# Kernel optimization log

Hardware: AMD Instinct MI355X
Metric: run time of the kernel (lower is better)

## Reference

```python
import jax, jax.numpy as jnp
import numpy as np

B = 32768
D_IN = 512
UNITS = 512


def setup_inputs() -> dict:
    key = jax.random.key(0)
    ks = jax.random.split(key, 12)
    s = 1.0 / np.sqrt(D_IN)
    sh = 1.0 / np.sqrt(UNITS)
    return {
        "inputs": jax.random.normal(ks[0], (B, D_IN), dtype=jnp.float32),
        "state": jax.random.normal(ks[1], (B, UNITS), dtype=jnp.float32),
        "att_score": jax.random.uniform(ks[2], (B, 1), dtype=jnp.float32),
        # update gate
        "Wu_x": jax.random.normal(ks[3], (D_IN, UNITS), dtype=jnp.float32) * s,
        "bu": jnp.zeros((UNITS,), dtype=jnp.float32),
        "Wu_h": jax.random.normal(ks[4], (UNITS, UNITS), dtype=jnp.float32) * sh,
        # reset gate
        "Wr_x": jax.random.normal(ks[5], (D_IN, UNITS), dtype=jnp.float32) * s,
        "br": jnp.zeros((UNITS,), dtype=jnp.float32),
        "Wr_h": jax.random.normal(ks[6], (UNITS, UNITS), dtype=jnp.float32) * sh,
        # candidate memory
        "Wc_x": jax.random.normal(ks[7], (D_IN, UNITS), dtype=jnp.float32) * s,
        "bc": jnp.zeros((UNITS,), dtype=jnp.float32),
        "Wc_h": jax.random.normal(ks[8], (UNITS, UNITS), dtype=jnp.float32) * sh,
    }


def reference(inputs, state, att_score, Wu_x, bu, Wu_h, Wr_x, br, Wr_h, Wc_x, bc, Wc_h):
    # u = sigmoid(Dense_act(x) + Dense_noact(h))
    u = jax.nn.sigmoid(inputs @ Wu_x + bu + state @ Wu_h)
    # r = sigmoid(Dense_act(x) + Dense_noact(h))
    r = jax.nn.sigmoid(inputs @ Wr_x + br + state @ Wr_h)
    # c = tanh(Dense_act(x) + r * Dense_noact(h))
    c = jnp.tanh(inputs @ Wc_x + bc + r * (state @ Wc_h))
    u_ = att_score * u  # [B,1] * [B,U] broadcast
    state_next = (1.0 - u_) * state + u_ * c
    return state_next
```

## Files before the change

### kernel.cpp

```cpp
#include <hip/hip_runtime.h>
#include <hip/hip_bf16.h>
#include <stdint.h>

#define B_ROWS 32768
#define DIM 512
#define THREADS 256
#define NKT 32
#define ABUF 8192
#define WBUF 12288
#define BUF (ABUF + WBUF)

typedef __attribute__((ext_vector_type(8))) __bf16 bf16x8;
typedef __attribute__((ext_vector_type(4))) float f32x4;
typedef __attribute__((ext_vector_type(4))) unsigned int uint4v;

__device__ static inline unsigned short f2bf(float f) {
    unsigned int u = __builtin_bit_cast(unsigned int, f);
    u += 0x7fffu + ((u >> 16) & 1u);
    return (unsigned short)(u >> 16);
}

__device__ static inline void load_lds_16B(const void* g, void* lds) {
    __builtin_amdgcn_global_load_lds(
        (const __attribute__((address_space(1))) unsigned int*)g,
        (__attribute__((address_space(3))) unsigned int*)lds,
        16, 0, 0);
}

__global__ void prep_weights(const float* __restrict__ Wu_x, const float* __restrict__ Wu_h,
                             const float* __restrict__ Wr_x, const float* __restrict__ Wr_h,
                             const float* __restrict__ Wc_x, const float* __restrict__ Wc_h,
                             unsigned short* __restrict__ Wt2) {
    __shared__ float tile[32][33];
    const int t = blockIdx.z;
    const int k0 = blockIdx.x * 32;
    const int n0 = blockIdx.y * 32;
    const float* Wx = (t == 0) ? Wu_x : (t == 1) ? Wr_x : Wc_x;
    const float* Wh = (t == 0) ? Wu_h : (t == 1) ? Wr_h : Wc_h;
    const int tid = threadIdx.x;
    const int c = tid & 31, r0 = tid >> 5;
#pragma unroll
    for (int i = 0; i < 4; ++i) {
        int kl = r0 + i * 8;
        int k = k0 + kl;
        int n = n0 + c;
        float v = (k < 512) ? Wx[(size_t)k * 512 + n] : Wh[(size_t)(k - 512) * 512 + n];
        tile[kl][c] = v;
    }
    __syncthreads();
    const int kt = k0 >> 5;
#pragma unroll
    for (int i = 0; i < 4; ++i) {
        int nl = r0 + i * 8;
        int kc = c;
        int n = n0 + nl;
        size_t base = (((size_t)kt * 3 + t) * 512 + n) * 64;
        *(unsigned short*)((char*)Wt2 + base + ((kc * 2) ^ (((n >> 1) & 3) << 4))) =
            f2bf(tile[kc][nl]);
    }
}

__global__ __launch_bounds__(THREADS, 2) void augru_main(
    const float* __restrict__ x, const float* __restrict__ h,
    const float* __restrict__ att, const unsigned short* __restrict__ Wt2,
    const float* __restrict__ bu, const float* __restrict__ br,
    const float* __restrict__ bc, float* __restrict__ out) {
    extern __shared__ char smem[];
    const int tid = threadIdx.x;
    const int lane = tid & 63;
    const int wid = tid >> 6;
    const int wm = wid >> 1;
    const int wn = wid & 1;
    const int id = blockIdx.x;
    const int wg = (id & 7) * 256 + (id >> 3);
    const int nb = wg & 7;
    const int mb = wg >> 3;
    const int cl = lane & 15;
    const int kg = lane >> 4;

    f32x4 accU[4][2], accR[4][2], accCx[4][2], accCh[4][2];
#pragma unroll
    for (int i = 0; i < 4; ++i)
#pragma unroll
        for (int j = 0; j < 2; ++j) {
            accU[i][j] = (f32x4)(0.f);
            accR[i][j] = (f32x4)(0.f);
            accCx[i][j] = (f32x4)(0.f);
            accCh[i][j] = (f32x4)(0.f);
        }

    const int rowb = wm * 64 + cl;
    const int aBase = rowb * 64 + ((kg * 16) ^ (((rowb >> 1) & 3) << 4));
    const int colb = wn * 32 + cl;
    const int wBase = ABUF + colb * 64 + ((kg * 16) ^ (((colb >> 1) & 3) << 4));

    const int arow = tid >> 1;
    const int ap = tid & 1;
    const int asw = ((arow >> 1) & 3) << 4;
    const int dsA0 = arow * 64 + ((ap * 32) ^ asw);
    const int dsA1 = arow * 64 + ((ap * 32 + 16) ^ asw);
    const float* pAx = x + (size_t)(mb * 128 + arow) * 512 + ap * 16;
    const float* pAh = h + (size_t)(mb * 128 + arow) * 512 - 512 + ap * 16;

    const char* gW0 = (const char*)Wt2 + ((size_t)nb * 64) * 64 + tid * 16;
    auto stageW = [&](int buf, int kt) {
        char* base = smem + buf * BUF;
        const char* gW = gW0 + (size_t)kt * (3 * 512 * 64);
#pragma unroll
        for (int t = 0; t < 3; ++t)
            load_lds_16B(gW + (size_t)t * (512 * 64),
                         base + ABUF + t * 4096 + wid * 1024);
    };

    f32x4 fa0, fa1, fa2, fa3;
    auto issueA = [&](int ktn) {
        const float* g = ((ktn < 16) ? pAx : pAh) + ktn * 32;
        asm volatile(
            "global_load_dwordx4 %0, %4, off\n\t"
            "global_load_dwordx4 %1, %4, off offset:16\n\t"
            "global_load_dwordx4 %2, %4, off offset:32\n\t"
            "global_load_dwordx4 %3, %4, off offset:48"
            : "=&v"(fa0), "=&v"(fa1), "=&v"(fa2), "=&v"(fa3)
            : "v"(g)
            : "memory");
    };

    auto cvt2 = [](float lo, float hi) {
        unsigned int r;
        asm("v_cvt_pk_bf16_f32 %0, %1, %2" : "=v"(r) : "v"(lo), "v"(hi));
        return r;
    };

    auto convertA = [&](int bufA, bool wLive) {
        if (wLive) asm volatile("s_waitcnt vmcnt(3)" ::: "memory");
        else       asm volatile("s_waitcnt vmcnt(0)" ::: "memory");
        __builtin_amdgcn_sched_barrier(0);
        uint4v q0, q1;
        q0.x = cvt2(fa0[0], fa0[1]); q0.y = cvt2(fa0[2], fa0[3]);
        q0.z = cvt2(fa1[0], fa1[1]); q0.w = cvt2(fa1[2], fa1[3]);
        q1.x = cvt2(fa2[0], fa2[1]); q1.y = cvt2(fa2[2], fa2[3]);
        q1.z = cvt2(fa3[0], fa3[1]); q1.w = cvt2(fa3[2], fa3[3]);
        char* base = smem + bufA * BUF;
        *(uint4v*)(base + dsA0) = q0;
        *(uint4v*)(base + dsA1) = q1;
    };

    stageW(0, 0);
    stageW(1, 1);
    stageW(2, 2);
    issueA(0);
    convertA(0, false);

    auto body = [&](int kt, int buf, int bufA, f32x4(&accC)[4][2]) {
        asm volatile("s_waitcnt lgkmcnt(0)" ::: "memory");
        __builtin_amdgcn_s_barrier();
        const bool doA = (kt + 1 < NKT);
        const bool doW = (kt + 3 < NKT);
        if (doA) issueA(kt + 1);
        if (doW) stageW((kt + 3) & 3, kt + 3);
        const char* aB = smem + buf * BUF;
        bf16x8 a[4], bb[3][2];
#pragma unroll
        for (int mi = 0; mi < 4; ++mi)
            a[mi] = __builtin_bit_cast(bf16x8,
                *(const uint4v*)(aB + aBase + mi * 1024));
#pragma unroll
        for (int t = 0; t < 3; ++t)
#pragma unroll
            for (int ni = 0; ni < 2; ++ni)
                bb[t][ni] = __builtin_bit_cast(bf16x8,
                    *(const uint4v*)(aB + wBase + t * 4096 + ni * 1024));
        __builtin_amdgcn_s_setprio(1);
#pragma unroll
        for (int ni = 0; ni < 2; ++ni) {
#pragma unroll
            for (int mi = 0; mi < 4; ++mi)
                accU[mi][ni] = __builtin_amdgcn_mfma_f32_16x16x32_bf16(
                    a[mi], bb[0][ni], accU[mi][ni], 0, 0, 0);
#pragma unroll
            for (int mi = 0; mi < 4; ++mi)
                accR[mi][ni] = __builtin_amdgcn_mfma_f32_16x16x32_bf16(
                    a[mi], bb[1][ni], accR[mi][ni], 0, 0, 0);
#pragma unroll
            for (int mi = 0; mi < 4; ++mi)
                accC[mi][ni] = __builtin_amdgcn_mfma_f32_16x16x32_bf16(
                    a[mi], bb[2][ni], accC[mi][ni], 0, 0, 0);
        }
        __builtin_amdgcn_s_setprio(0);
        if (doA) convertA(bufA, doW);
    };

    for (int g = 0; g < 4; ++g) {
        const int k0 = g * 4;
        body(k0 + 0, 0, 1, accCx);
        body(k0 + 1, 1, 2, accCx);
        body(k0 + 2, 2, 3, accCx);
        body(k0 + 3, 3, 0, accCx);
    }
    for (int g = 4; g < 8; ++g) {
        const int k0 = g * 4;
        body(k0 + 0, 0, 1, accCh);
        body(k0 + 1, 1, 2, accCh);
        body(k0 + 2, 2, 3, accCh);
        body(k0 + 3, 3, 0, accCh);
    }

#pragma unroll
    for (int ni = 0; ni < 2; ++ni) {
        const int col = nb * 64 + wn * 32 + ni * 16 + cl;
        const float bU = bu[col];
        const float bR = br[col];
        const float bC = bc[col];
#pragma unroll
        for (int mi = 0; mi < 4; ++mi) {
#pragma unroll
            for (int j = 0; j < 4; ++j) {
                const int row = mb * 128 + wm * 64 + mi * 16 + kg * 4 + j;
                const float up = accU[mi][ni][j] + bU;
                const float rp = accR[mi][ni][j] + bR;
                const float u = 1.f / (1.f + __expf(-up));
                const float r = 1.f / (1.f + __expf(-rp));
                const float cpre = accCx[mi][ni][j] + bC + r * accCh[mi][ni][j];
                const float e = __expf(-2.f * cpre);
                const float cc = (1.f - e) / (1.f + e);
                const float aa = att[row];
                const float hv = h[(size_t)row * 512 + col];
                const float u_ = aa * u;
                out[(size_t)row * 512 + col] = (1.f - u_) * hv + u_ * cc;
            }
        }
    }
}

extern "C" void kernel_launch(void* const* d_in, const int* in_sizes, int n_in,
                              void* d_out, int out_size, void* d_ws, size_t ws_size,
                              hipStream_t stream) {
    const float* x    = (const float*)d_in[0];
    const float* h    = (const float*)d_in[1];
    const float* att  = (const float*)d_in[2];
    const float* Wu_x = (const float*)d_in[3];
    const float* bu   = (const float*)d_in[4];
    const float* Wu_h = (const float*)d_in[5];
    const float* Wr_x = (const float*)d_in[6];
    const float* br   = (const float*)d_in[7];
    const float* Wr_h = (const float*)d_in[8];
    const float* Wc_x = (const float*)d_in[9];
    const float* bc   = (const float*)d_in[10];
    const float* Wc_h = (const float*)d_in[11];
    unsigned short* Wt2 = (unsigned short*)d_ws;
    float* out = (float*)d_out;

    prep_weights<<<dim3(32, 16, 3), 256, 0, stream>>>(Wu_x, Wu_h, Wr_x, Wr_h, Wc_x, Wc_h, Wt2);

    hipFuncSetAttribute((const void*)augru_main,
                        hipFuncAttributeMaxDynamicSharedMemorySize, 4 * BUF);
    augru_main<<<dim3(2048), THREADS, 4 * BUF, stream>>>(
        x, h, att, Wt2, bu, br, bc, out);
}
```

Measured before the change: 139.0 us.

## Deepen A-operand prefetch to two tiles ahead and split LDS layout

Measured after the change: 142.2 us (median of 2 runs). +2.3%, slower.

```diff
diff --git a/kernel.cpp b/kernel.cpp
--- a/kernel.cpp
+++ b/kernel.cpp
@@ -6,9 +6,10 @@
 #define DIM 512
 #define THREADS 256
 #define NKT 32
-#define ABUF 8192
-#define WBUF 12288
-#define BUF (ABUF + WBUF)
+#define ASLOT 8192
+#define WBUFB 12288
+#define WBASE 16384
+#define LDS_TOTAL (WBASE + 4 * WBUFB)
 
 typedef __attribute__((ext_vector_type(8))) __bf16 bf16x8;
 typedef __attribute__((ext_vector_type(4))) float f32x4;
@@ -92,7 +93,7 @@
     const int rowb = wm * 64 + cl;
     const int aBase = rowb * 64 + ((kg * 16) ^ (((rowb >> 1) & 3) << 4));
     const int colb = wn * 32 + cl;
-    const int wBase = ABUF + colb * 64 + ((kg * 16) ^ (((colb >> 1) & 3) << 4));
+    const int wBase = WBASE + colb * 64 + ((kg * 16) ^ (((colb >> 1) & 3) << 4));
 
     const int arow = tid >> 1;
     const int ap = tid & 1;
@@ -104,23 +105,23 @@
 
     const char* gW0 = (const char*)Wt2 + ((size_t)nb * 64) * 64 + tid * 16;
     auto stageW = [&](int buf, int kt) {
-        char* base = smem + buf * BUF;
+        char* base = smem + WBASE + buf * WBUFB;
         const char* gW = gW0 + (size_t)kt * (3 * 512 * 64);
 #pragma unroll
         for (int t = 0; t < 3; ++t)
             load_lds_16B(gW + (size_t)t * (512 * 64),
-                         base + ABUF + t * 4096 + wid * 1024);
-    };
-
-    f32x4 fa0, fa1, fa2, fa3;
-    auto issueA = [&](int ktn) {
+                         base + t * 4096 + wid * 1024);
+    };
+
+    f32x4 fa[2][4];
+    auto issueA = [&](int ktn, int p) {
         const float* g = ((ktn < 16) ? pAx : pAh) + ktn * 32;
         asm volatile(
             "global_load_dwordx4 %0, %4, off\n\t"
             "global_load_dwordx4 %1, %4, off offset:16\n\t"
             "global_load_dwordx4 %2, %4, off offset:32\n\t"
             "global_load_dwordx4 %3, %4, off offset:48"
-            : "=&v"(fa0), "=&v"(fa1), "=&v"(fa2), "=&v"(fa3)
+            : "=&v"(fa[p][0]), "=&v"(fa[p][1]), "=&v"(fa[p][2]), "=&v"(fa[p][3])
             : "v"(g)
             : "memory");
     };
@@ -131,16 +132,14 @@
         return r;
     };
 
-    auto convertA = [&](int bufA, bool wLive) {
-        if (wLive) asm volatile("s_waitcnt vmcnt(3)" ::: "memory");
-        else       asm volatile("s_waitcnt vmcnt(0)" ::: "memory");
+    auto convertA = [&](int p, int slot) {
         __builtin_amdgcn_sched_barrier(0);
         uint4v q0, q1;
-        q0.x = cvt2(fa0[0], fa0[1]); q0.y = cvt2(fa0[2], fa0[3]);
-        q0.z = cvt2(fa1[0], fa1[1]); q0.w = cvt2(fa1[2], fa1[3]);
-        q1.x = cvt2(fa2[0], fa2[1]); q1.y = cvt2(fa2[2], fa2[3]);
-        q1.z = cvt2(fa3[0], fa3[1]); q1.w = cvt2(fa3[2], fa3[3]);
-        char* base = smem + bufA * BUF;
+        q0.x = cvt2(fa[p][0][0], fa[p][0][1]); q0.y = cvt2(fa[p][0][2], fa[p][0][3]);
+        q0.z = cvt2(fa[p][1][0], fa[p][1][1]); q0.w = cvt2(fa[p][1][2], fa[p][1][3]);
+        q1.x = cvt2(fa[p][2][0], fa[p][2][1]); q1.y = cvt2(fa[p][2][2], fa[p][2][3]);
+        q1.z = cvt2(fa[p][3][0], fa[p][3][1]); q1.w = cvt2(fa[p][3][2], fa[p][3][3]);
+        char* base = smem + slot * ASLOT;
         *(uint4v*)(base + dsA0) = q0;
         *(uint4v*)(base + dsA1) = q1;
     };
@@ -148,28 +147,32 @@
     stageW(0, 0);
     stageW(1, 1);
     stageW(2, 2);
-    issueA(0);
-    convertA(0, false);
-
-    auto body = [&](int kt, int buf, int bufA, f32x4(&accC)[4][2]) {
-        asm volatile("s_waitcnt lgkmcnt(0)" ::: "memory");
+    issueA(0, 0);
+    asm volatile("s_waitcnt vmcnt(0)" ::: "memory");
+    convertA(0, 0);
+    issueA(1, 1);
+
+    auto body = [&](int kt, int bufW, int slotA, int wait, f32x4(&accC)[4][2]) {
+        if (wait == 3) asm volatile("s_waitcnt vmcnt(3) lgkmcnt(0)" ::: "memory");
+        else           asm volatile("s_waitcnt vmcnt(0) lgkmcnt(0)" ::: "memory");
         __builtin_amdgcn_s_barrier();
-        const bool doA = (kt + 1 < NKT);
-        const bool doW = (kt + 3 < NKT);
-        if (doA) issueA(kt + 1);
-        if (doW) stageW((kt + 3) & 3, kt + 3);
-        const char* aB = smem + buf * BUF;
+        const int p = slotA;
+        if (kt + 2 < NKT) issueA(kt + 2, p);
+        if (kt + 3 < NKT) stageW((kt + 3) & 3, kt + 3);
+        const char* aS = smem + slotA * ASLOT;
+        const char* wB = smem + bufW * WBUFB;
         bf16x8 a[4], bb[3][2];
 #pragma unroll
         for (int mi = 0; mi < 4; ++mi)
             a[mi] = __builtin_bit_cast(bf16x8,
-                *(const uint4v*)(aB + aBase + mi * 1024));
+                *(const uint4v*)(aS + aBase + mi * 1024));
 #pragma unroll
         for (int t = 0; t < 3; ++t)
 #pragma unroll
             for (int ni = 0; ni < 2; ++ni)
                 bb[t][ni] = __builtin_bit_cast(bf16x8,
-                    *(const uint4v*)(aB + wBase + t * 4096 + ni * 1024));
+                    *(const uint4v*)(wB + wBase + t * 4096 + ni * 1024));
+        if (kt + 1 < NKT) convertA(p ^ 1, slotA ^ 1);
         __builtin_amdgcn_s_setprio(1);
 #pragma unroll
         for (int ni = 0; ni < 2; ++ni) {
@@ -187,23 +190,30 @@
                     a[mi], bb[2][ni], accC[mi][ni], 0, 0, 0);
         }
         __builtin_amdgcn_s_setprio(0);
-        if (doA) convertA(bufA, doW);
-    };
-
-    for (int g = 0; g < 4; ++g) {
+    };
+
+    body(0, 0, 0, 0, accCx);
+    body(1, 1, 1, 3, accCx);
+    body(2, 2, 0, 3, accCx);
+    body(3, 3, 1, 3, accCx);
+    for (int g = 1; g < 4; ++g) {
         const int k0 = g * 4;
-        body(k0 + 0, 0, 1, accCx);
-        body(k0 + 1, 1, 2, accCx);
-        body(k0 + 2, 2, 3, accCx);
-        body(k0 + 3, 3, 0, accCx);
-    }
-    for (int g = 4; g < 8; ++g) {
+        body(k0 + 0, 0, 0, 3, accCx);
+        body(k0 + 1, 1, 1, 3, accCx);
+        body(k0 + 2, 2, 0, 3, accCx);
+        body(k0 + 3, 3, 1, 3, accCx);
+    }
+    for (int g = 4; g < 7; ++g) {
         const int k0 = g * 4;
-        body(k0 + 0, 0, 1, accCh);
-        body(k0 + 1, 1, 2, accCh);
-        body(k0 + 2, 2, 3, accCh);
-        body(k0 + 3, 3, 0, accCh);
-    }
+        body(k0 + 0, 0, 0, 3, accCh);
+        body(k0 + 1, 1, 1, 3, accCh);
+        body(k0 + 2, 2, 0, 3, accCh);
+        body(k0 + 3, 3, 1, 3, accCh);
+    }
+    body(28, 0, 0, 3, accCh);
+    body(29, 1, 1, 3, accCh);
+    body(30, 2, 0, 0, accCh);
+    body(31, 3, 1, 0, accCh);
 
 #pragma unroll
     for (int ni = 0; ni < 2; ++ni) {
@@ -253,7 +263,7 @@
     prep_weights<<<dim3(32, 16, 3), 256, 0, stream>>>(Wu_x, Wu_h, Wr_x, Wr_h, Wc_x, Wc_h, Wt2);
 
     hipFuncSetAttribute((const void*)augru_main,
-                        hipFuncAttributeMaxDynamicSharedMemorySize, 4 * BUF);
-    augru_main<<<dim3(2048), THREADS, 4 * BUF, stream>>>(
+                        hipFuncAttributeMaxDynamicSharedMemorySize, LDS_TOTAL);
+    augru_main<<<dim3(2048), THREADS, LDS_TOTAL, stream>>>(
         x, h, att, Wt2, bu, br, bc, out);
 }
```

## Stage fp32 activations to LDS directly, load weights straight into registers

Applied to the files above, without the earlier changes.

Measured after the change: 158.8 us. 1.14x slower.

```diff
diff --git a/kernel.cpp b/kernel.cpp
--- a/kernel.cpp
+++ b/kernel.cpp
@@ -6,9 +6,8 @@
 #define DIM 512
 #define THREADS 256
 #define NKT 32
-#define ABUF 8192
-#define WBUF 12288
-#define BUF (ABUF + WBUF)
+#define ASLOT 16384
+#define LDS_TOTAL (3 * ASLOT)
 
 typedef __attribute__((ext_vector_type(8))) __bf16 bf16x8;
 typedef __attribute__((ext_vector_type(4))) float f32x4;
@@ -54,9 +53,7 @@
         int nl = r0 + i * 8;
         int kc = c;
         int n = n0 + nl;
-        size_t base = (((size_t)kt * 3 + t) * 512 + n) * 64;
-        *(unsigned short*)((char*)Wt2 + base + ((kc * 2) ^ (((n >> 1) & 3) << 4))) =
-            f2bf(tile[kc][nl]);
+        Wt2[(((size_t)kt * 3 + t) * 512 + n) * 32 + kc] = f2bf(tile[kc][nl]);
     }
 }
 
@@ -89,40 +86,30 @@
             accCh[i][j] = (f32x4)(0.f);
         }
 
-    const int rowb = wm * 64 + cl;
-    const int aBase = rowb * 64 + ((kg * 16) ^ (((rowb >> 1) & 3) << 4));
-    const int colb = wn * 32 + cl;
-    const int wBase = ABUF + colb * 64 + ((kg * 16) ^ (((colb >> 1) & 3) << 4));
-
-    const int arow = tid >> 1;
-    const int ap = tid & 1;
-    const int asw = ((arow >> 1) & 3) << 4;
-    const int dsA0 = arow * 64 + ((ap * 32) ^ asw);
-    const int dsA1 = arow * 64 + ((ap * 32 + 16) ^ asw);
-    const float* pAx = x + (size_t)(mb * 128 + arow) * 512 + ap * 16;
-    const float* pAh = h + (size_t)(mb * 128 + arow) * 512 - 512 + ap * 16;
-
-    const char* gW0 = (const char*)Wt2 + ((size_t)nb * 64) * 64 + tid * 16;
-    auto stageW = [&](int buf, int kt) {
-        char* base = smem + buf * BUF;
-        const char* gW = gW0 + (size_t)kt * (3 * 512 * 64);
+    const int arow_l = lane >> 3;
+    const int ag = lane & 7;
+    const unsigned aoffBase =
+        (unsigned)(mb * 128 + wid * 32 + arow_l) * 2048
+        + (unsigned)((ag * 16) ^ (arow_l << 4));
+    auto stageA = [&](int slot, int ktn) {
+        const char* bp = (ktn < 16) ? (const char*)x : (const char*)h;
+        const unsigned ko = (unsigned)(ktn & 15) * 128;
+        char* ldsb = smem + slot * ASLOT + wid * 4096;
+#pragma unroll
+        for (int q = 0; q < 4; ++q)
+            load_lds_16B(bp + aoffBase + q * 16384 + ko, ldsb + q * 1024);
+    };
+
+    const char* gW = (const char*)Wt2
+        + (size_t)((nb * 64 + wn * 32 + cl) * 64 + kg * 16);
+    bf16x8 bbA[3][2], bbB[3][2];
+    auto loadW = [&](bf16x8(&dst)[3][2], int ktn) {
+        const char* p = gW + (size_t)ktn * 98304;
 #pragma unroll
         for (int t = 0; t < 3; ++t)
-            load_lds_16B(gW + (size_t)t * (512 * 64),
-                         base + ABUF + t * 4096 + wid * 1024);
-    };
-
-    f32x4 fa0, fa1, fa2, fa3;
-    auto issueA = [&](int ktn) {
-        const float* g = ((ktn < 16) ? pAx : pAh) + ktn * 32;
-        asm volatile(
-            "global_load_dwordx4 %0, %4, off\n\t"
-            "global_load_dwordx4 %1, %4, off offset:16\n\t"
-            "global_load_dwordx4 %2, %4, off offset:32\n\t"
-            "global_load_dwordx4 %3, %4, off offset:48"
-            : "=&v"(fa0), "=&v"(fa1), "=&v"(fa2), "=&v"(fa3)
-            : "v"(g)
-            : "memory");
+#pragma unroll
+            for (int ni = 0; ni < 2; ++ni)
+                dst[t][ni] = *(const bf16x8*)(p + t * 32768 + ni * 1024);
     };
 
     auto cvt2 = [](float lo, float hi) {
@@ -131,79 +118,70 @@
         return r;
     };
 
-    auto convertA = [&](int bufA, bool wLive) {
-        if (wLive) asm volatile("s_waitcnt vmcnt(3)" ::: "memory");
-        else       asm volatile("s_waitcnt vmcnt(0)" ::: "memory");
+    const int s7 = cl & 7;
+    const int aRd1 = (wm * 64 + cl) * 128 + (((kg * 2) ^ s7) * 16);
+    const int aRd2 = (wm * 64 + cl) * 128 + (((kg * 2 + 1) ^ s7) * 16);
+    auto readA = [&](int slot, int mi) {
+        const char* p = smem + slot * ASLOT + mi * 2048;
+        f32x4 lo = *(const f32x4*)(p + aRd1);
+        f32x4 hi = *(const f32x4*)(p + aRd2);
+        uint4v q;
+        q.x = cvt2(lo[0], lo[1]); q.y = cvt2(lo[2], lo[3]);
+        q.z = cvt2(hi[0], hi[1]); q.w = cvt2(hi[2], hi[3]);
+        return __builtin_bit_cast(bf16x8, q);
+    };
+
+    stageA(0, 0);
+    stageA(1, 1);
+    loadW(bbA, 0);
+
+    auto body = [&](int kt, bf16x8(&cur)[3][2], bf16x8(&nxt)[3][2],
+                    f32x4(&accC)[4][2]) {
+        asm volatile("s_waitcnt vmcnt(0)" ::: "memory");
+        __builtin_amdgcn_s_barrier();
+        if (kt + 2 < NKT) stageA((kt + 2) % 3, kt + 2);
+        if (kt + 1 < NKT) loadW(nxt, kt + 1);
         __builtin_amdgcn_sched_barrier(0);
-        uint4v q0, q1;
-        q0.x = cvt2(fa0[0], fa0[1]); q0.y = cvt2(fa0[2], fa0[3]);
-        q0.z = cvt2(fa1[0], fa1[1]); q0.w = cvt2(fa1[2], fa1[3]);
-        q1.x = cvt2(fa2[0], fa2[1]); q1.y = cvt2(fa2[2], fa2[3]);
-        q1.z = cvt2(fa3[0], fa3[1]); q1.w = cvt2(fa3[2], fa3[3]);
-        char* base = smem + bufA * BUF;
-        *(uint4v*)(base + dsA0) = q0;
-        *(uint4v*)(base + dsA1) = q1;
-    };
-
-    stageW(0, 0);
-    stageW(1, 1);
-    stageW(2, 2);
-    issueA(0);
-    convertA(0, false);
-
-    auto body = [&](int kt, int buf, int bufA, f32x4(&accC)[4][2]) {
-        asm volatile("s_waitcnt lgkmcnt(0)" ::: "memory");
-        __builtin_amdgcn_s_barrier();
-        const bool doA = (kt + 1 < NKT);
-        const bool doW = (kt + 3 < NKT);
-        if (doA) issueA(kt + 1);
-        if (doW) stageW((kt + 3) & 3, kt + 3);
-        const char* aB = smem + buf * BUF;
-        bf16x8 a[4], bb[3][2];
+        const int slot = kt % 3;
+        bf16x8 a[4];
 #pragma unroll
         for (int mi = 0; mi < 4; ++mi)
-            a[mi] = __builtin_bit_cast(bf16x8,
-                *(const uint4v*)(aB + aBase + mi * 1024));
-#pragma unroll
-        for (int t = 0; t < 3; ++t)
-#pragma unroll
-            for (int ni = 0; ni < 2; ++ni)
-                bb[t][ni] = __builtin_bit_cast(bf16x8,
-                    *(const uint4v*)(aB + wBase + t * 4096 + ni * 1024));
+            a[mi] = readA(slot, mi);
         __builtin_amdgcn_s_setprio(1);
 #pragma unroll
         for (int ni = 0; ni < 2; ++ni) {
 #pragma unroll
             for (int mi = 0; mi < 4; ++mi)
                 accU[mi][ni] = __builtin_amdgcn_mfma_f32_16x16x32_bf16(
-                    a[mi], bb[0][ni], accU[mi][ni], 0, 0, 0);
+                    a[mi], cur[0][ni], accU[mi][ni], 0, 0, 0);
 #pragma unroll
             for (int mi = 0; mi < 4; ++mi)
                 accR[mi][ni] = __builtin_amdgcn_mfma_f32_16x16x32_bf16(
-                    a[mi], bb[1][ni], accR[mi][ni], 0, 0, 0);
+                    a[mi], cur[1][ni], accR[mi][ni], 0, 0, 0);
 #pragma unroll
             for (int mi = 0; mi < 4; ++mi)
                 accC[mi][ni] = __builtin_amdgcn_mfma_f32_16x16x32_bf16(
-                    a[mi], bb[2][ni], accC[mi][ni], 0, 0, 0);
+                    a[mi], cur[2][ni], accC[mi][ni], 0, 0, 0);
         }
         __builtin_amdgcn_s_setprio(0);
-        if (doA) convertA(bufA, doW);
-    };
-
-    for (int g = 0; g < 4; ++g) {
-        const int k0 = g * 4;
-        body(k0 + 0, 0, 1, accCx);
-        body(k0 + 1, 1, 2, accCx);
-        body(k0 + 2, 2, 3, accCx);
-        body(k0 + 3, 3, 0, accCx);
-    }
-    for (int g = 4; g < 8; ++g) {
-        const int k0 = g * 4;
-        body(k0 + 0, 0, 1, accCh);
-        body(k0 + 1, 1, 2, accCh);
-        body(k0 + 2, 2, 3, accCh);
-        body(k0 + 3, 3, 0, accCh);
-    }
+    };
+
+    body(0, bbA, bbB, accCx);  body(1, bbB, bbA, accCx);
+    body(2, bbA, bbB, accCx);  body(3, bbB, bbA, accCx);
+    body(4, bbA, bbB, accCx);  body(5, bbB, bbA, accCx);
+    body(6, bbA, bbB, accCx);  body(7, bbB, bbA, accCx);
+    body(8, bbA, bbB, accCx);  body(9, bbB, bbA, accCx);
+    body(10, bbA, bbB, accCx); body(11, bbB, bbA, accCx);
+    body(12, bbA, bbB, accCx); body(13, bbB, bbA, accCx);
+    body(14, bbA, bbB, accCx); body(15, bbB, bbA, accCx);
+    body(16, bbA, bbB, accCh); body(17, bbB, bbA, accCh);
+    body(18, bbA, bbB, accCh); body(19, bbB, bbA, accCh);
+    body(20, bbA, bbB, accCh); body(21, bbB, bbA, accCh);
+    body(22, bbA, bbB, accCh); body(23, bbB, bbA, accCh);
+    body(24, bbA, bbB, accCh); body(25, bbB, bbA, accCh);
+    body(26, bbA, bbB, accCh); body(27, bbB, bbA, accCh);
+    body(28, bbA, bbB, accCh); body(29, bbB, bbA, accCh);
+    body(30, bbA, bbB, accCh); body(31, bbB, bbA, accCh);
 
 #pragma unroll
     for (int ni = 0; ni < 2; ++ni) {
@@ -253,7 +231,7 @@
     prep_weights<<<dim3(32, 16, 3), 256, 0, stream>>>(Wu_x, Wu_h, Wr_x, Wr_h, Wc_x, Wc_h, Wt2);
 
     hipFuncSetAttribute((const void*)augru_main,
-                        hipFuncAttributeMaxDynamicSharedMemorySize, 4 * BUF);
-    augru_main<<<dim3(2048), THREADS, 4 * BUF, stream>>>(
+                        hipFuncAttributeMaxDynamicSharedMemorySize, LDS_TOTAL);
+    augru_main<<<dim3(2048), THREADS, LDS_TOTAL, stream>>>(
         x, h, att, Wt2, bu, br, bc, out);
 }
```
